# Optimization experiments

Measured on AMD Instinct MI355X. Metric: run time of the kernel, lower is better.

## Reference

```python
import jax, jax.numpy as jnp
import numpy as np

EPS = 1e-6
GROUPS = 32
SCALE = 1.0 / np.float32(512.0) ** 0.5


def setup_inputs() -> dict:
    key = jax.random.key(0)
    ks = jax.random.split(key, 8)
    b, c, h, w = 4, 512, 64, 64
    std = 0.02
    return {
        "x": jax.random.normal(ks[0], (b, c, h, w), dtype=jnp.float32),
        "gamma": jnp.ones((c,), jnp.float32),
        "beta": jnp.zeros((c,), jnp.float32),
        "wq_w": jax.random.normal(ks[1], (c, c), jnp.float32) * std,
        "wq_b": jax.random.normal(ks[2], (c,), jnp.float32) * std,
        "wk_w": jax.random.normal(ks[3], (c, c), jnp.float32) * std,
        "wk_b": jax.random.normal(ks[4], (c,), jnp.float32) * std,
        "wv_w": jax.random.normal(ks[5], (c, c), jnp.float32) * std,
        "wv_b": jax.random.normal(ks[6], (c,), jnp.float32) * std,
        "out_w": jax.random.normal(ks[7], (c, c), jnp.float32) * std,
        "out_b": jnp.zeros((c,), jnp.float32),
    }


def reference(x, gamma, beta, wq_w, wq_b, wk_w, wk_b, wv_w, wv_b, out_w, out_b):
    b, c, h, w = x.shape
    # GroupNorm(32 groups, eps=1e-6, affine)
    xg = x.reshape(b, GROUPS, c // GROUPS, h, w)
    mean = xg.mean(axis=(2, 3, 4), keepdims=True)
    var = ((xg - mean) ** 2).mean(axis=(2, 3, 4), keepdims=True)
    xn = ((xg - mean) * jax.lax.rsqrt(var + EPS)).reshape(b, c, h, w)
    xn = xn * gamma[None, :, None, None] + beta[None, :, None, None]
    # flatten spatial -> tokens: [b, N, c]
    t = xn.reshape(b, c, h * w).transpose(0, 2, 1)
    q = t @ wq_w.T + wq_b
    k = t @ wk_w.T + wk_b
    v = t @ wv_w.T + wv_b
    scores = jnp.einsum('bnc,bmc->bnm', q, k) * SCALE  # [b, N, N]
    attn = jax.nn.softmax(scores, axis=2)
    o = jnp.einsum('bnm,bmc->bnc', attn, v)
    o = o @ out_w.T + out_b
    return o.transpose(0, 2, 1).reshape(b, c, h, w) + x
```

## Files before the change

kernel.cpp:

```cpp
#include <hip/hip_runtime.h>
#include <hip/hip_fp8.h>

typedef unsigned short u16;
typedef unsigned char u8;
typedef unsigned int u32;
typedef short bf16x8 __attribute__((ext_vector_type(8)));
typedef float f32x4 __attribute__((ext_vector_type(4)));
typedef u16 u16x4 __attribute__((ext_vector_type(4)));

#define SCALE_Q 0.044194173824159216f

#define BAR() asm volatile("s_waitcnt lgkmcnt(0)\n\ts_barrier" ::: "memory")

__device__ __forceinline__ u16 f2b(float f){
  unsigned u = __float_as_uint(f);
  u += 0x7fffu + ((u >> 16) & 1u);
  return (u16)(u >> 16);
}

__device__ __forceinline__ u8 f2e4(float f){
  return __hip_fp8_e4m3(f).__x;
}

__device__ __forceinline__ void gload16(const void* g, void* l){
  __builtin_amdgcn_global_load_lds(
      (const __attribute__((address_space(1))) void*)g,
      (__attribute__((address_space(3))) void*)l, 16, 0, 0);
}

__device__ __forceinline__ float qsum16(float v){
  v += __shfl_xor(v, 1); v += __shfl_xor(v, 2);
  v += __shfl_xor(v, 4); v += __shfl_xor(v, 8);
  return v;
}

__global__ __launch_bounds__(256) void gn_stats(const float* __restrict__ x,
                                                float* __restrict__ stats){
  int bg = blockIdx.x;
  const float4* p4 = (const float4*)(x + (size_t)bg * 65536);
  float s = 0.f, ss = 0.f;
  for (int i = threadIdx.x; i < 16384; i += 256){
    float4 v = p4[i];
    s  += v.x + v.y + v.z + v.w;
    ss += v.x*v.x + v.y*v.y + v.z*v.z + v.w*v.w;
  }
  for (int off = 32; off; off >>= 1){
    s  += __shfl_down(s, off);
    ss += __shfl_down(ss, off);
  }
  __shared__ float as_[4], bs_[4];
  int wid = threadIdx.x >> 6, lid = threadIdx.x & 63;
  if (lid == 0){ as_[wid] = s; bs_[wid] = ss; }
  __syncthreads();
  if (threadIdx.x == 0){
    float S = as_[0]+as_[1]+as_[2]+as_[3], SS = bs_[0]+bs_[1]+bs_[2]+bs_[3];
    float mean = S * (1.f/65536.f);
    float var  = SS * (1.f/65536.f) - mean*mean;
    stats[2*bg]   = mean;
    stats[2*bg+1] = rsqrtf(var + 1e-6f);
  }
}

__global__ __launch_bounds__(256) void gn_apply_T(const float* __restrict__ x,
                                                  const float* __restrict__ stats,
                                                  const float* __restrict__ gamma,
                                                  const float* __restrict__ beta,
                                                  u16* __restrict__ t){
  __shared__ float tile[32][33];
  int nb = blockIdx.x, cb = blockIdx.y, b = blockIdx.z;
  int tx = threadIdx.x & 31, ty = threadIdx.x >> 5;
  int n0 = nb * 32, c0 = cb * 32;
  #pragma unroll
  for (int i = 0; i < 4; i++){
    int ch = c0 + ty + i*8;
    float mean = stats[2*((b<<5) + (ch>>4))];
    float rstd = stats[2*((b<<5) + (ch>>4)) + 1];
    float v = x[(((size_t)b*512 + ch) << 12) + n0 + tx];
    tile[ty + i*8][tx] = (v - mean) * rstd * gamma[ch] + beta[ch];
  }
  __syncthreads();
  #pragma unroll
  for (int i = 0; i < 4; i++){
    int n = n0 + ty + i*8;
    int ch = c0 + tx;
    t[((size_t)((b<<12) + n))*512 + ch] = f2b(tile[tx][ty + i*8]);
  }
}

__global__ __launch_bounds__(256) void w2bf(const float* __restrict__ a,
                                            const float* __restrict__ b,
                                            const float* __restrict__ c,
                                            const float* __restrict__ d,
                                            u16* __restrict__ o){
  int idx = blockIdx.x * 256 + threadIdx.x;
  int which = idx >> 16;
  const float4* src = (const float4*)(which == 0 ? a : which == 1 ? b : which == 2 ? c : d);
  float4 v = src[idx & 65535];
  u16x4 pk;
  pk.x = f2b(v.x); pk.y = f2b(v.y); pk.z = f2b(v.z); pk.w = f2b(v.w);
  *(u16x4*)(o + (size_t)idx*4) = pk;
}

__global__ __launch_bounds__(256, 2) void qkv_gemm(const u16* __restrict__ A,
                                                   const u16* __restrict__ Wcat,
                                                   const float* __restrict__ qbias,
                                                   const float* __restrict__ kbias,
                                                   const float* __restrict__ vbias,
                                                   u8* __restrict__ qo,
                                                   u8* __restrict__ ko,
                                                   u8* __restrict__ vo){
  __shared__ __align__(16) u16 SMEM[8192];
  u16* As = SMEM;
  u16* Bs = SMEM + 4096;
  const int t = threadIdx.x;
  const int w = t >> 6, ln = t & 63;
  const int wr = w >> 1, wc = w & 1;
  const int q4 = ln >> 4, l15 = ln & 15;
  const int y = blockIdx.y;
  const int mat = y >> 2, yb = y & 3;
  const int row0 = blockIdx.x * 128;
  const u16* Ab = A    + (size_t)row0 * 512;
  const u16* Bb = Wcat + (size_t)y * 128 * 512;
  f32x4 acc[4][4];
  #pragma unroll
  for (int i = 0; i < 4; i++)
    #pragma unroll
    for (int j = 0; j < 4; j++){
      acc[i][j][0]=0.f; acc[i][j][1]=0.f; acc[i][j][2]=0.f; acc[i][j][3]=0.f;
    }
  for (int kt = 0; kt < 16; ++kt){
    #pragma unroll
    for (int i = 0; i < 2; i++){
      int idx = i*256 + t;
      gload16(Ab + (size_t)(idx>>2)*512 + kt*32 + (idx&3)*8, As + (size_t)idx*8);
      gload16(Bb + (size_t)(idx>>2)*512 + kt*32 + (idx&3)*8, Bs + (size_t)idx*8);
    }
    __syncthreads();
    bf16x8 af[4], bf[4];
    #pragma unroll
    for (int mt = 0; mt < 4; mt++)
      af[mt] = *(const bf16x8*)(As + (wr*64 + mt*16 + l15)*32 + q4*8);
    #pragma unroll
    for (int nt = 0; nt < 4; nt++)
      bf[nt] = *(const bf16x8*)(Bs + (wc*64 + nt*16 + l15)*32 + q4*8);
    #pragma unroll
    for (int mt = 0; mt < 4; mt++)
      #pragma unroll
      for (int nt = 0; nt < 4; nt++)
        acc[mt][nt] = __builtin_amdgcn_mfma_f32_16x16x32_bf16(af[mt], bf[nt], acc[mt][nt], 0, 0, 0);
    __syncthreads();
  }
  const int bb = row0 >> 12;
  const int tile0 = (row0 >> 6) & 63;
  const int col0 = yb*128 + wc*64;
  u8* Ls = (u8*)SMEM;

  if (mat == 0){
    #pragma unroll
    for (int nt = 0; nt < 4; nt++){
      int n = col0 + nt*16 + l15;
      float bv = qbias[n];
      #pragma unroll
      for (int mt = 0; mt < 4; mt++){
        int m0 = row0 + wr*64 + mt*16 + q4*4;
        #pragma unroll
        for (int r = 0; r < 4; r++)
          qo[(size_t)(m0 + r)*512 + n] = f2e4(acc[mt][nt][r] + bv);
      }
    }
  } else if (mat == 1){
    #pragma unroll
    for (int nt = 0; nt < 4; nt++){
      int n = col0 + nt*16 + l15;
      float bv = kbias[n];
      int ksl = wc*2 + (nt >> 1);
      int c3  = ((nt & 1)*2 + (l15 >> 3));
      #pragma unroll
      for (int mt = 0; mt < 4; mt++){
        #pragma unroll
        for (int r = 0; r < 4; r++){
          int kr = mt*16 + q4*4 + r;
          int chunk = c3 ^ ((kr >> 2) & 3);
          Ls[(wr*4 + ksl)*2048 + kr*32 + chunk*8 + (l15 & 7)] = f2e4(acc[mt][nt][r] + bv);
        }
      }
    }
    __syncthreads();
    #pragma unroll
    for (int i = 0; i < 4; i++){
      int ci = i*256 + t;
      int ri = ci >> 7, t2 = ri >> 2, ksl2 = ri & 3;
      u8* dst = ko + ((size_t)(bb*64 + tile0 + t2))*32768
                   + (size_t)(yb*4 + ksl2)*2048 + (size_t)(ci & 127)*16;
      *(float4*)dst = *(const float4*)(Ls + (size_t)ci*16);
    }
  } else {
    #pragma unroll
    for (int nt = 0; nt < 4; nt++){
      int n = col0 + nt*16 + l15;
      float bv = vbias[n];
      int nl = n & 127;
      #pragma unroll
      for (int mt = 0; mt < 4; mt++){
        int kv = mt*16 + q4*4;
        u32 pk = (u32)f2e4(acc[mt][nt][0] + bv)
               | ((u32)f2e4(acc[mt][nt][1] + bv) << 8)
               | ((u32)f2e4(acc[mt][nt][2] + bv) << 16)
               | ((u32)f2e4(acc[mt][nt][3] + bv) << 24);
        int phys = (kv >> 3) ^ (n & 7);
        *(u32*)(Ls + wr*8192 + nl*64 + phys*8 + (kv & 4)) = pk;
      }
    }
    __syncthreads();
    #pragma unroll
    for (int i = 0; i < 4; i++){
      int ci = i*256 + t;
      int t2 = ci >> 9;
      u8* dst = vo + ((size_t)(bb*64 + tile0 + t2))*32768
                   + (size_t)yb*8192 + (size_t)(ci & 511)*16;
      *(float4*)dst = *(const float4*)(Ls + (size_t)ci*16);
    }
  }
}

__global__ __launch_bounds__(256, 2) void out_gemm(const u16* __restrict__ A,
                                                   const u16* __restrict__ Bw,
                                                   const float* __restrict__ bias,
                                                   float* __restrict__ out,
                                                   const float* __restrict__ resid){
  __shared__ __align__(16) u16 As[128*32];
  __shared__ __align__(16) u16 Bs[128*32];
  const int t = threadIdx.x;
  const int w = t >> 6, ln = t & 63;
  const int wr = w >> 1, wc = w & 1;
  const int q4 = ln >> 4, l15 = ln & 15;
  const u16* Ab = A  + (size_t)blockIdx.x * 128 * 512;
  const u16* Bb = Bw + (size_t)blockIdx.y * 128 * 512;
  f32x4 acc[4][4];
  #pragma unroll
  for (int i = 0; i < 4; i++)
    #pragma unroll
    for (int j = 0; j < 4; j++){
      acc[i][j][0]=0.f; acc[i][j][1]=0.f; acc[i][j][2]=0.f; acc[i][j][3]=0.f;
    }
  for (int kt = 0; kt < 16; ++kt){
    #pragma unroll
    for (int i = 0; i < 2; i++){
      int idx = i*256 + t;
      gload16(Ab + (size_t)(idx>>2)*512 + kt*32 + (idx&3)*8, As + (size_t)idx*8);
      gload16(Bb + (size_t)(idx>>2)*512 + kt*32 + (idx&3)*8, Bs + (size_t)idx*8);
    }
    __syncthreads();
    bf16x8 af[4], bf[4];
    #pragma unroll
    for (int mt = 0; mt < 4; mt++)
      af[mt] = *(const bf16x8*)(As + (wr*64 + mt*16 + l15)*32 + q4*8);
    #pragma unroll
    for (int nt = 0; nt < 4; nt++)
      bf[nt] = *(const bf16x8*)(Bs + (wc*64 + nt*16 + l15)*32 + q4*8);
    #pragma unroll
    for (int mt = 0; mt < 4; mt++)
      #pragma unroll
      for (int nt = 0; nt < 4; nt++)
        acc[mt][nt] = __builtin_amdgcn_mfma_f32_16x16x32_bf16(af[mt], bf[nt], acc[mt][nt], 0, 0, 0);
    __syncthreads();
  }
  const int row0 = blockIdx.x*128 + wr*64;
  const int col0 = blockIdx.y*128 + wc*64;
  #pragma unroll
  for (int nt = 0; nt < 4; nt++){
    int n = col0 + nt*16 + l15;
    float bv = bias[n];
    #pragma unroll
    for (int mt = 0; mt < 4; mt++){
      int m0 = row0 + mt*16 + q4*4;
      int bb = m0 >> 12, tok = m0 & 4095;
      size_t base = (((size_t)(bb*512 + n)) << 12) + tok;
      float4 xr = *(const float4*)(resid + base);
      float4 ov;
      ov.x = acc[mt][nt][0] + bv + xr.x;
      ov.y = acc[mt][nt][1] + bv + xr.y;
      ov.z = acc[mt][nt][2] + bv + xr.z;
      ov.w = acc[mt][nt][3] + bv + xr.w;
      *(float4*)(out + base) = ov;
    }
  }
}

__global__ __launch_bounds__(256, 2) void attn_fwd(const u8* __restrict__ q,
                                                   const u8* __restrict__ kt,
                                                   const u8* __restrict__ vt,
                                                   u16* __restrict__ outO){
  __shared__ __align__(16) u8 Kb[2][32768];
  __shared__ __align__(16) u8 Pb[32*72];
  __shared__ __align__(16) float lL[64];

  const int t = threadIdx.x, w = t >> 6, ln = t & 63;
  const int q4 = ln >> 4, l15 = ln & 15;
  const int rt = w >> 1, chh = w & 1;
  const int b = blockIdx.y, q0 = blockIdx.x * 32;
  const u8* kbase = kt + ((size_t)b << 21);
  const u8* vbase = vt + ((size_t)b << 21);

  long qf[16];
  {
    const u8* qr = q + (size_t)((b<<12) + q0 + rt*16 + l15) * 512;
    #pragma unroll
    for (int ks = 0; ks < 16; ks++) qf[ks] = *(const long*)(qr + ks*32 + q4*8);
  }
  f32x4 oacc[2][8];
  #pragma unroll
  for (int i = 0; i < 2; i++)
    #pragma unroll
    for (int j = 0; j < 8; j++){
      oacc[i][j][0]=0.f; oacc[i][j][1]=0.f; oacc[i][j][2]=0.f; oacc[i][j][3]=0.f;
    }
  f32x4 lrow; lrow[0]=0.f; lrow[1]=0.f; lrow[2]=0.f; lrow[3]=0.f;

  const int kr0 = chh*32 + l15,  kr1 = chh*32 + 16 + l15;
  const int ko0 = kr0*32 + ((q4 ^ ((kr0 >> 2) & 3)) << 3);
  const int ko1 = kr1*32 + ((q4 ^ ((kr1 >> 2) & 3)) << 3);

  #pragma unroll
  for (int i = 0; i < 8; i++){
    int ci = i*256 + t;
    gload16(kbase + (size_t)ci*16, &Kb[0][ci*16]);
  }
  __syncthreads();

  #pragma unroll 1
  for (int j = 0; j < 64; ++j){
    {
      const u8* kn = kbase + ((size_t)((j + 1) & 63) << 15);
      u8* kd = Kb[(j + 1) & 1];
      #pragma unroll
      for (int i = 0; i < 8; i++){
        int ci = i*256 + t;
        gload16(kn + (size_t)ci*16, kd + ci*16);
      }
    }
    long vf0[8], vf1[8];
    {
      const u8* vtile = vbase + ((size_t)j << 15);
      #pragma unroll
      for (int ct = 0; ct < 8; ct++){
        int ch = 128*w + ct*16 + l15;
        int swz = ch & 7;
        const u8* vr = vtile + (size_t)ch*64;
        vf0[ct] = *(const long*)(vr + ((q4 ^ swz) << 3));
        vf1[ct] = *(const long*)(vr + (((4 + q4) ^ swz) << 3));
      }
    }
    const u8* Kp = Kb[j & 1];
    f32x4 sA0, sA1, sB0, sB1;
    sA0[0]=0.f;sA0[1]=0.f;sA0[2]=0.f;sA0[3]=0.f;
    sA1[0]=0.f;sA1[1]=0.f;sA1[2]=0.f;sA1[3]=0.f;
    sB0[0]=0.f;sB0[1]=0.f;sB0[2]=0.f;sB0[3]=0.f;
    sB1[0]=0.f;sB1[1]=0.f;sB1[2]=0.f;sB1[3]=0.f;
    #pragma unroll
    for (int k2 = 0; k2 < 8; k2++){
      const u8* e0 = Kp + (2*k2)*2048;
      const u8* e1 = Kp + (2*k2 + 1)*2048;
      long ka0 = *(const long*)(e0 + ko0);
      long kb0 = *(const long*)(e0 + ko1);
      long ka1 = *(const long*)(e1 + ko0);
      long kb1 = *(const long*)(e1 + ko1);
      sA0 = __builtin_amdgcn_mfma_f32_16x16x32_fp8_fp8(qf[2*k2],   ka0, sA0, 0, 0, 0);
      sB0 = __builtin_amdgcn_mfma_f32_16x16x32_fp8_fp8(qf[2*k2],   kb0, sB0, 0, 0, 0);
      sA1 = __builtin_amdgcn_mfma_f32_16x16x32_fp8_fp8(qf[2*k2+1], ka1, sA1, 0, 0, 0);
      sB1 = __builtin_amdgcn_mfma_f32_16x16x32_fp8_fp8(qf[2*k2+1], kb1, sB1, 0, 0, 0);
    }
    #pragma unroll
    for (int r = 0; r < 4; r++){
      float e0 = __expf((sA0[r] + sA1[r]) * SCALE_Q);
      float e1 = __expf((sB0[r] + sB1[r]) * SCALE_Q);
      lrow[r] += e0 + e1;
      int row = rt*16 + q4*4 + r;
      Pb[row*72 + chh*32 + l15]      = f2e4(e0);
      Pb[row*72 + chh*32 + 16 + l15] = f2e4(e1);
    }
    BAR();
    {
      long pf00 = *(const long*)(Pb + l15*72 + q4*8);
      long pf01 = *(const long*)(Pb + l15*72 + 32 + q4*8);
      long pf10 = *(const long*)(Pb + (16 + l15)*72 + q4*8);
      long pf11 = *(const long*)(Pb + (16 + l15)*72 + 32 + q4*8);
      #pragma unroll
      for (int ct = 0; ct < 8; ct++){
        f32x4 a0 = oacc[0][ct], a1 = oacc[1][ct];
        a0 = __builtin_amdgcn_mfma_f32_16x16x32_fp8_fp8(pf00, vf0[ct], a0, 0, 0, 0);
        a1 = __builtin_amdgcn_mfma_f32_16x16x32_fp8_fp8(pf10, vf0[ct], a1, 0, 0, 0);
        a0 = __builtin_amdgcn_mfma_f32_16x16x32_fp8_fp8(pf01, vf1[ct], a0, 0, 0, 0);
        a1 = __builtin_amdgcn_mfma_f32_16x16x32_fp8_fp8(pf11, vf1[ct], a1, 0, 0, 0);
        oacc[0][ct] = a0; oacc[1][ct] = a1;
      }
    }
    __syncthreads();
  }

  {
    f32x4 ls;
    #pragma unroll
    for (int r = 0; r < 4; r++) ls[r] = qsum16(lrow[r]);
    if (l15 == 0) *(f32x4*)&lL[chh*32 + rt*16 + q4*4] = ls;
  }
  __syncthreads();
  #pragma unroll
  for (int rr = 0; rr < 2; rr++){
    #pragma unroll
    for (int r = 0; r < 4; r++){
      int row = rr*16 + q4*4 + r;
      float inv = 1.f / (lL[row] + lL[32 + row]);
      u16* op = outO + ((size_t)b << 21) + (size_t)(q0 + row)*512 + 128*w + l15;
      #pragma unroll
      for (int ct = 0; ct < 8; ct++)
        op[ct*16] = f2b(oacc[rr][ct][r] * inv);
    }
  }
}

extern "C" void kernel_launch(void* const* d_in, const int* in_sizes, int n_in,
                              void* d_out, int out_size, void* d_ws, size_t ws_size,
                              hipStream_t stream){
  const float* x     = (const float*)d_in[0];
  const float* gamma = (const float*)d_in[1];
  const float* beta  = (const float*)d_in[2];
  const float* wq_w  = (const float*)d_in[3];
  const float* wq_b  = (const float*)d_in[4];
  const float* wk_w  = (const float*)d_in[5];
  const float* wk_b  = (const float*)d_in[6];
  const float* wv_w  = (const float*)d_in[7];
  const float* wv_b  = (const float*)d_in[8];
  const float* out_w = (const float*)d_in[9];
  const float* out_b = (const float*)d_in[10];

  char* ws = (char*)d_ws;
  float* stats = (float*)ws;
  u16* tbuf = (u16*)(ws + 4096);
  size_t off = 4096 + (size_t)16*1024*1024;
  u16* Wcat = (u16*)(ws + off); off += (size_t)4*512*512*2;
  u8*  qb   = (u8*)(ws + off);  off += (size_t)16*1024*1024;
  u8*  ktb  = (u8*)(ws + off);  off += (size_t)16*1024*1024;
  u8*  vtb  = (u8*)(ws + off);  off += (size_t)16*1024*1024;

  gn_stats<<<128, 256, 0, stream>>>(x, stats);
  gn_apply_T<<<dim3(128, 16, 4), 256, 0, stream>>>(x, stats, gamma, beta, tbuf);
  w2bf<<<1024, 256, 0, stream>>>(wq_w, wk_w, wv_w, out_w, Wcat);
  u16* Wo = Wcat + 3*512*512;
  qkv_gemm<<<dim3(128, 12), 256, 0, stream>>>(tbuf, Wcat, wq_b, wk_b, wv_b,
                                              qb, ktb, vtb);
  attn_fwd<<<dim3(128, 4), 256, 0, stream>>>(qb, ktb, vtb, tbuf);
  out_gemm<<<dim3(128, 4), 256, 0, stream>>>(tbuf, Wo, out_b, (float*)d_out, x);
}
```

Measured before the change: 323.9 us.

## Software-pipeline attention loop: overlap PV of previous tile with QK of current

Restructures the attention inner loop into a two-stage software pipeline. The P@V product for tile j-1 runs right after the QK MFMAs for tile j, and P and V fragments are double-buffered so only one barrier per iteration remains. The loop is unrolled by two through a macro, and MFMA sections are wrapped in s_setprio raises. This aims to remove the mid-iteration barrier stall and hide exp/softmax latency behind matrix work. The cost is higher register pressure from the extra V fragment buffers, which could spill at the two-blocks-per-SM launch bound.

```diff
diff --git a/kernel.cpp b/kernel.cpp
--- a/kernel.cpp
+++ b/kernel.cpp
@@ -9,8 +9,6 @@
 typedef u16 u16x4 __attribute__((ext_vector_type(4)));
 
 #define SCALE_Q 0.044194173824159216f
-
-#define BAR() asm volatile("s_waitcnt lgkmcnt(0)\n\ts_barrier" ::: "memory")
 
 __device__ __forceinline__ u16 f2b(float f){
   unsigned u = __float_as_uint(f);
@@ -287,12 +285,84 @@
   }
 }
 
+#define AITER(J, PCUR, PPRV, VN0, VN1, VP0, VP1, KCUR, KNXT)                  \
+  {                                                                           \
+                 \
+    if ((J) < 63){                                                            \
+      const u8* kn = kbase + ((size_t)((J) + 1) << 15);                       \
+      _Pragma("unroll")                                                       \
+      for (int i = 0; i < 8; i++){                                            \
+        int ci = i*256 + t;                                                   \
+        gload16(kn + (size_t)ci*16, &Kb[KNXT][ci*16]);                        \
+      }                                                                       \
+    }                                                                         \
+        \
+    {                                                                         \
+      const u8* vtile = vbase + ((size_t)(J) << 15);                          \
+      _Pragma("unroll")                                                       \
+      for (int ct = 0; ct < 8; ct++){                                         \
+        int ch = 128*w + ct*16 + l15;                                         \
+        int swz = ch & 7;                                                     \
+        const u8* vr = vtile + (size_t)ch*64;                                 \
+        VN0[ct] = *(const long*)(vr + ((q4 ^ swz) << 3));                     \
+        VN1[ct] = *(const long*)(vr + (((4 + q4) ^ swz) << 3));               \
+      }                                                                       \
+    }                                                                         \
+                             \
+    const u8* Kp = Kb[KCUR];                                                  \
+    f32x4 sA0 = {0.f,0.f,0.f,0.f}, sA1 = {0.f,0.f,0.f,0.f};                   \
+    f32x4 sB0 = {0.f,0.f,0.f,0.f}, sB1 = {0.f,0.f,0.f,0.f};                   \
+    __builtin_amdgcn_s_setprio(1);                                            \
+    _Pragma("unroll")                                                         \
+    for (int k2 = 0; k2 < 8; k2++){                                           \
+      const u8* e0 = Kp + (2*k2)*2048;                                        \
+      const u8* e1 = Kp + (2*k2 + 1)*2048;                                    \
+      long ka0 = *(const long*)(e0 + ko0);                                    \
+      long kb0 = *(const long*)(e0 + ko1);                                    \
+      long ka1 = *(const long*)(e1 + ko0);                                    \
+      long kb1 = *(const long*)(e1 + ko1);                                    \
+      sA0 = __builtin_amdgcn_mfma_f32_16x16x32_fp8_fp8(qf[2*k2],   ka0, sA0, 0, 0, 0); \
+      sB0 = __builtin_amdgcn_mfma_f32_16x16x32_fp8_fp8(qf[2*k2],   kb0, sB0, 0, 0, 0); \
+      sA1 = __builtin_amdgcn_mfma_f32_16x16x32_fp8_fp8(qf[2*k2+1], ka1, sA1, 0, 0, 0); \
+      sB1 = __builtin_amdgcn_mfma_f32_16x16x32_fp8_fp8(qf[2*k2+1], kb1, sB1, 0, 0, 0); \
+    }                                                                         \
+      \
+    if ((J) > 0){                                                             \
+      long pf00 = *(const long*)((PPRV) + l15*72 + q4*8);                     \
+      long pf01 = *(const long*)((PPRV) + l15*72 + 32 + q4*8);                \
+      long pf10 = *(const long*)((PPRV) + (16 + l15)*72 + q4*8);              \
+      long pf11 = *(const long*)((PPRV) + (16 + l15)*72 + 32 + q4*8);         \
+      _Pragma("unroll")                                                       \
+      for (int ct = 0; ct < 8; ct++){                                         \
+        f32x4 a0 = oacc[0][ct], a1 = oacc[1][ct];                             \
+        a0 = __builtin_amdgcn_mfma_f32_16x16x32_fp8_fp8(pf00, VP0[ct], a0, 0, 0, 0); \
+        a1 = __builtin_amdgcn_mfma_f32_16x16x32_fp8_fp8(pf10, VP0[ct], a1, 0, 0, 0); \
+        a0 = __builtin_amdgcn_mfma_f32_16x16x32_fp8_fp8(pf01, VP1[ct], a0, 0, 0, 0); \
+        a1 = __builtin_amdgcn_mfma_f32_16x16x32_fp8_fp8(pf11, VP1[ct], a1, 0, 0, 0); \
+        oacc[0][ct] = a0; oacc[1][ct] = a1;                                   \
+      }                                                                       \
+    }                                                                         \
+    __builtin_amdgcn_s_setprio(0);                                            \
+              \
+    _Pragma("unroll")                                                         \
+    for (int r = 0; r < 4; r++){                                              \
+      float e0 = __expf((sA0[r] + sA1[r]) * SCALE_Q);                         \
+      float e1 = __expf((sB0[r] + sB1[r]) * SCALE_Q);                         \
+      lrow[r] += e0 + e1;                                                     \
+      int row = rt*16 + q4*4 + r;                                             \
+      (PCUR)[row*72 + chh*32 + l15]      = f2e4(e0);                          \
+      (PCUR)[row*72 + chh*32 + 16 + l15] = f2e4(e1);                          \
+    }                                                                         \
+           \
+    __syncthreads();                                                          \
+  }
+
 __global__ __launch_bounds__(256, 2) void attn_fwd(const u8* __restrict__ q,
                                                    const u8* __restrict__ kt,
                                                    const u8* __restrict__ vt,
                                                    u16* __restrict__ outO){
   __shared__ __align__(16) u8 Kb[2][32768];
-  __shared__ __align__(16) u8 Pb[32*72];
+  __shared__ __align__(16) u8 Pb[2][32*72];
   __shared__ __align__(16) float lL[64];
 
   const int t = threadIdx.x, w = t >> 6, ln = t & 63;
@@ -328,74 +398,29 @@
   }
   __syncthreads();
 
+  long vA0[8], vA1[8], vB0[8], vB1[8];
+
   #pragma unroll 1
-  for (int j = 0; j < 64; ++j){
-    {
-      const u8* kn = kbase + ((size_t)((j + 1) & 63) << 15);
-      u8* kd = Kb[(j + 1) & 1];
-      #pragma unroll
-      for (int i = 0; i < 8; i++){
-        int ci = i*256 + t;
-        gload16(kn + (size_t)ci*16, kd + ci*16);
-      }
-    }
-    long vf0[8], vf1[8];
-    {
-      const u8* vtile = vbase + ((size_t)j << 15);
-      #pragma unroll
-      for (int ct = 0; ct < 8; ct++){
-        int ch = 128*w + ct*16 + l15;
-        int swz = ch & 7;
-        const u8* vr = vtile + (size_t)ch*64;
-        vf0[ct] = *(const long*)(vr + ((q4 ^ swz) << 3));
-        vf1[ct] = *(const long*)(vr + (((4 + q4) ^ swz) << 3));
-      }
-    }
-    const u8* Kp = Kb[j & 1];
-    f32x4 sA0, sA1, sB0, sB1;
-    sA0[0]=0.f;sA0[1]=0.f;sA0[2]=0.f;sA0[3]=0.f;
-    sA1[0]=0.f;sA1[1]=0.f;sA1[2]=0.f;sA1[3]=0.f;
-    sB0[0]=0.f;sB0[1]=0.f;sB0[2]=0.f;sB0[3]=0.f;
-    sB1[0]=0.f;sB1[1]=0.f;sB1[2]=0.f;sB1[3]=0.f;
-    #pragma unroll
-    for (int k2 = 0; k2 < 8; k2++){
-      const u8* e0 = Kp + (2*k2)*2048;
-      const u8* e1 = Kp + (2*k2 + 1)*2048;
-      long ka0 = *(const long*)(e0 + ko0);
-      long kb0 = *(const long*)(e0 + ko1);
-      long ka1 = *(const long*)(e1 + ko0);
-      long kb1 = *(const long*)(e1 + ko1);
-      sA0 = __builtin_amdgcn_mfma_f32_16x16x32_fp8_fp8(qf[2*k2],   ka0, sA0, 0, 0, 0);
-      sB0 = __builtin_amdgcn_mfma_f32_16x16x32_fp8_fp8(qf[2*k2],   kb0, sB0, 0, 0, 0);
-      sA1 = __builtin_amdgcn_mfma_f32_16x16x32_fp8_fp8(qf[2*k2+1], ka1, sA1, 0, 0, 0);
-      sB1 = __builtin_amdgcn_mfma_f32_16x16x32_fp8_fp8(qf[2*k2+1], kb1, sB1, 0, 0, 0);
-    }
-    #pragma unroll
-    for (int r = 0; r < 4; r++){
-      float e0 = __expf((sA0[r] + sA1[r]) * SCALE_Q);
-      float e1 = __expf((sB0[r] + sB1[r]) * SCALE_Q);
-      lrow[r] += e0 + e1;
-      int row = rt*16 + q4*4 + r;
-      Pb[row*72 + chh*32 + l15]      = f2e4(e0);
-      Pb[row*72 + chh*32 + 16 + l15] = f2e4(e1);
-    }
-    BAR();
-    {
-      long pf00 = *(const long*)(Pb + l15*72 + q4*8);
-      long pf01 = *(const long*)(Pb + l15*72 + 32 + q4*8);
-      long pf10 = *(const long*)(Pb + (16 + l15)*72 + q4*8);
-      long pf11 = *(const long*)(Pb + (16 + l15)*72 + 32 + q4*8);
-      #pragma unroll
-      for (int ct = 0; ct < 8; ct++){
-        f32x4 a0 = oacc[0][ct], a1 = oacc[1][ct];
-        a0 = __builtin_amdgcn_mfma_f32_16x16x32_fp8_fp8(pf00, vf0[ct], a0, 0, 0, 0);
-        a1 = __builtin_amdgcn_mfma_f32_16x16x32_fp8_fp8(pf10, vf0[ct], a1, 0, 0, 0);
-        a0 = __builtin_amdgcn_mfma_f32_16x16x32_fp8_fp8(pf01, vf1[ct], a0, 0, 0, 0);
-        a1 = __builtin_amdgcn_mfma_f32_16x16x32_fp8_fp8(pf11, vf1[ct], a1, 0, 0, 0);
-        oacc[0][ct] = a0; oacc[1][ct] = a1;
-      }
-    }
-    __syncthreads();
+  for (int j = 0; j < 64; j += 2){
+    AITER(j,     Pb[0], Pb[1], vA0, vA1, vB0, vB1, 0, 1);
+    AITER(j + 1, Pb[1], Pb[0], vB0, vB1, vA0, vA1, 1, 0);
+  }
+
+  {
+    const u8* PP = Pb[1];
+    long pf00 = *(const long*)(PP + l15*72 + q4*8);
+    long pf01 = *(const long*)(PP + l15*72 + 32 + q4*8);
+    long pf10 = *(const long*)(PP + (16 + l15)*72 + q4*8);
+    long pf11 = *(const long*)(PP + (16 + l15)*72 + 32 + q4*8);
+    #pragma unroll
+    for (int ct = 0; ct < 8; ct++){
+      f32x4 a0 = oacc[0][ct], a1 = oacc[1][ct];
+      a0 = __builtin_amdgcn_mfma_f32_16x16x32_fp8_fp8(pf00, vB0[ct], a0, 0, 0, 0);
+      a1 = __builtin_amdgcn_mfma_f32_16x16x32_fp8_fp8(pf10, vB0[ct], a1, 0, 0, 0);
+      a0 = __builtin_amdgcn_mfma_f32_16x16x32_fp8_fp8(pf01, vB1[ct], a0, 0, 0, 0);
+      a1 = __builtin_amdgcn_mfma_f32_16x16x32_fp8_fp8(pf11, vB1[ct], a1, 0, 0, 0);
+      oacc[0][ct] = a0; oacc[1][ct] = a1;
+    }
   }
 
   {
```

Measured after the change: 384.4 us. 1.19x slower.

## Software-pipeline attention loop: overlap QK of tile j with PV of tile j-1

Applied to the files above, without the earlier changes.

Restructures the attention main loop so each iteration computes QK scores for the current key tile while running the PV MFMAs on the probabilities from the previous tile, using a double-buffered P array in LDS. This removes one of the two barriers per iteration and lets exp/softmax work overlap MFMA work from another stage. A tail block handles the last PV tile, and s_setprio raises wave priority around the MFMA section. The trade-off is higher register pressure from holding V fragments and score accumulators together, plus a slightly larger LDS footprint.

```diff
diff --git a/kernel.cpp b/kernel.cpp
--- a/kernel.cpp
+++ b/kernel.cpp
@@ -9,8 +9,6 @@
 typedef u16 u16x4 __attribute__((ext_vector_type(4)));
 
 #define SCALE_Q 0.044194173824159216f
-
-#define BAR() asm volatile("s_waitcnt lgkmcnt(0)\n\ts_barrier" ::: "memory")
 
 __device__ __forceinline__ u16 f2b(float f){
   unsigned u = __float_as_uint(f);
@@ -292,7 +290,7 @@
                                                    const u8* __restrict__ vt,
                                                    u16* __restrict__ outO){
   __shared__ __align__(16) u8 Kb[2][32768];
-  __shared__ __align__(16) u8 Pb[32*72];
+  __shared__ __align__(16) u8 Pb[2][32*72];
   __shared__ __align__(16) float lL[64];
 
   const int t = threadIdx.x, w = t >> 6, ln = t & 63;
@@ -330,8 +328,8 @@
 
   #pragma unroll 1
   for (int j = 0; j < 64; ++j){
-    {
-      const u8* kn = kbase + ((size_t)((j + 1) & 63) << 15);
+    if (j < 63){
+      const u8* kn = kbase + ((size_t)(j + 1) << 15);
       u8* kd = Kb[(j + 1) & 1];
       #pragma unroll
       for (int i = 0; i < 8; i++){
@@ -340,8 +338,8 @@
       }
     }
     long vf0[8], vf1[8];
-    {
-      const u8* vtile = vbase + ((size_t)j << 15);
+    if (j > 0){
+      const u8* vtile = vbase + ((size_t)(j - 1) << 15);
       #pragma unroll
       for (int ct = 0; ct < 8; ct++){
         int ch = 128*w + ct*16 + l15;
@@ -357,6 +355,7 @@
     sA1[0]=0.f;sA1[1]=0.f;sA1[2]=0.f;sA1[3]=0.f;
     sB0[0]=0.f;sB0[1]=0.f;sB0[2]=0.f;sB0[3]=0.f;
     sB1[0]=0.f;sB1[1]=0.f;sB1[2]=0.f;sB1[3]=0.f;
+    __builtin_amdgcn_s_setprio(1);
     #pragma unroll
     for (int k2 = 0; k2 < 8; k2++){
       const u8* e0 = Kp + (2*k2)*2048;
@@ -370,21 +369,12 @@
       sA1 = __builtin_amdgcn_mfma_f32_16x16x32_fp8_fp8(qf[2*k2+1], ka1, sA1, 0, 0, 0);
       sB1 = __builtin_amdgcn_mfma_f32_16x16x32_fp8_fp8(qf[2*k2+1], kb1, sB1, 0, 0, 0);
     }
-    #pragma unroll
-    for (int r = 0; r < 4; r++){
-      float e0 = __expf((sA0[r] + sA1[r]) * SCALE_Q);
-      float e1 = __expf((sB0[r] + sB1[r]) * SCALE_Q);
-      lrow[r] += e0 + e1;
-      int row = rt*16 + q4*4 + r;
-      Pb[row*72 + chh*32 + l15]      = f2e4(e0);
-      Pb[row*72 + chh*32 + 16 + l15] = f2e4(e1);
-    }
-    BAR();
-    {
-      long pf00 = *(const long*)(Pb + l15*72 + q4*8);
-      long pf01 = *(const long*)(Pb + l15*72 + 32 + q4*8);
-      long pf10 = *(const long*)(Pb + (16 + l15)*72 + q4*8);
-      long pf11 = *(const long*)(Pb + (16 + l15)*72 + 32 + q4*8);
+    if (j > 0){
+      const u8* Pp = Pb[(j - 1) & 1];
+      long pf00 = *(const long*)(Pp + l15*72 + q4*8);
+      long pf01 = *(const long*)(Pp + l15*72 + 32 + q4*8);
+      long pf10 = *(const long*)(Pp + (16 + l15)*72 + q4*8);
+      long pf11 = *(const long*)(Pp + (16 + l15)*72 + 32 + q4*8);
       #pragma unroll
       for (int ct = 0; ct < 8; ct++){
         f32x4 a0 = oacc[0][ct], a1 = oacc[1][ct];
@@ -395,7 +385,44 @@
         oacc[0][ct] = a0; oacc[1][ct] = a1;
       }
     }
-    __syncthreads();
+    __builtin_amdgcn_s_setprio(0);
+    #pragma unroll
+    for (int r = 0; r < 4; r++){
+      float e0 = __expf((sA0[r] + sA1[r]) * SCALE_Q);
+      float e1 = __expf((sB0[r] + sB1[r]) * SCALE_Q);
+      lrow[r] += e0 + e1;
+      int row = rt*16 + q4*4 + r;
+      Pb[j & 1][row*72 + chh*32 + l15]      = f2e4(e0);
+      Pb[j & 1][row*72 + chh*32 + 16 + l15] = f2e4(e1);
+    }
+    __syncthreads();
+  }
+
+  {
+    const u8* vtile = vbase + ((size_t)63 << 15);
+    long vf0[8], vf1[8];
+    #pragma unroll
+    for (int ct = 0; ct < 8; ct++){
+      int ch = 128*w + ct*16 + l15;
+      int swz = ch & 7;
+      const u8* vr = vtile + (size_t)ch*64;
+      vf0[ct] = *(const long*)(vr + ((q4 ^ swz) << 3));
+      vf1[ct] = *(const long*)(vr + (((4 + q4) ^ swz) << 3));
+    }
+    const u8* Pp = Pb[1];
+    long pf00 = *(const long*)(Pp + l15*72 + q4*8);
+    long pf01 = *(const long*)(Pp + l15*72 + 32 + q4*8);
+    long pf10 = *(const long*)(Pp + (16 + l15)*72 + q4*8);
+    long pf11 = *(const long*)(Pp + (16 + l15)*72 + 32 + q4*8);
+    #pragma unroll
+    for (int ct = 0; ct < 8; ct++){
+      f32x4 a0 = oacc[0][ct], a1 = oacc[1][ct];
+      a0 = __builtin_amdgcn_mfma_f32_16x16x32_fp8_fp8(pf00, vf0[ct], a0, 0, 0, 0);
+      a1 = __builtin_amdgcn_mfma_f32_16x16x32_fp8_fp8(pf10, vf0[ct], a1, 0, 0, 0);
+      a0 = __builtin_amdgcn_mfma_f32_16x16x32_fp8_fp8(pf01, vf1[ct], a0, 0, 0, 0);
+      a1 = __builtin_amdgcn_mfma_f32_16x16x32_fp8_fp8(pf11, vf1[ct], a1, 0, 0, 0);
+      oacc[0][ct] = a0; oacc[1][ct] = a1;
+    }
   }
 
   {
```

Measured after the change: 338.0 us. 4.4% more time.

## Warp-specialize attention into score and PV wave groups with software pipelining

Applied to the files above, without the earlier changes.

The attention kernel moves to 512 threads and splits them into two roles. Four waves compute QK^T scores and exp for the current 128-key tile, and four waves run the PV MFMAs for the previous tile from a double-buffered P tile, so softmax and the two matmuls overlap across tiles. K tiles double in size to 64 KB per buffer, which halves the loop trip count. P is packed to fp8 four values at a time with cvt_pk, and s_setprio is raised around MFMA bursts. In exchange the kernel uses much more LDS (about 137 KB), which may limit occupancy to one block per CU despite the launch bound of two, and the two roles can become imbalanced.

```diff
diff --git a/kernel.cpp b/kernel.cpp
--- a/kernel.cpp
+++ b/kernel.cpp
@@ -10,8 +10,6 @@
 
 #define SCALE_Q 0.044194173824159216f
 
-#define BAR() asm volatile("s_waitcnt lgkmcnt(0)\n\ts_barrier" ::: "memory")
-
 __device__ __forceinline__ u16 f2b(float f){
   unsigned u = __float_as_uint(f);
   u += 0x7fffu + ((u >> 16) & 1u);
@@ -22,16 +20,21 @@
   return __hip_fp8_e4m3(f).__x;
 }
 
+__device__ __forceinline__ u32 pk4e4(float e0, float e1, float e2, float e3){
+#if defined(__has_builtin) && __has_builtin(__builtin_amdgcn_cvt_pk_fp8_f32)
+  int pk = __builtin_amdgcn_cvt_pk_fp8_f32(e0, e1, 0, false);
+  pk = __builtin_amdgcn_cvt_pk_fp8_f32(e2, e3, pk, true);
+  return (u32)pk;
+#else
+  return (u32)f2e4(e0) | ((u32)f2e4(e1) << 8)
+       | ((u32)f2e4(e2) << 16) | ((u32)f2e4(e3) << 24);
+#endif
+}
+
 __device__ __forceinline__ void gload16(const void* g, void* l){
   __builtin_amdgcn_global_load_lds(
       (const __attribute__((address_space(1))) void*)g,
       (__attribute__((address_space(3))) void*)l, 16, 0, 0);
-}
-
-__device__ __forceinline__ float qsum16(float v){
-  v += __shfl_xor(v, 1); v += __shfl_xor(v, 2);
-  v += __shfl_xor(v, 4); v += __shfl_xor(v, 8);
-  return v;
 }
 
 __global__ __launch_bounds__(256) void gn_stats(const float* __restrict__ x,
@@ -287,134 +290,210 @@
   }
 }
 
-__global__ __launch_bounds__(256, 2) void attn_fwd(const u8* __restrict__ q,
+#define PSTR 140
+__global__ __launch_bounds__(512, 2) void attn_fwd(const u8* __restrict__ q,
                                                    const u8* __restrict__ kt,
                                                    const u8* __restrict__ vt,
                                                    u16* __restrict__ outO){
-  __shared__ __align__(16) u8 Kb[2][32768];
-  __shared__ __align__(16) u8 Pb[32*72];
+  __shared__ __align__(16) u8 Kb[2][65536];
+  __shared__ __align__(16) u8 Pb[2][32*PSTR];
   __shared__ __align__(16) float lL[64];
 
   const int t = threadIdx.x, w = t >> 6, ln = t & 63;
   const int q4 = ln >> 4, l15 = ln & 15;
-  const int rt = w >> 1, chh = w & 1;
   const int b = blockIdx.y, q0 = blockIdx.x * 32;
   const u8* kbase = kt + ((size_t)b << 21);
   const u8* vbase = vt + ((size_t)b << 21);
+  const bool isS = (w < 4);
+  const int rt = w & 1, kvH = w >> 1;
+  const int wp = w & 3, ch0 = wp * 128;
 
   long qf[16];
-  {
+  int ko0, ko1, ko2, ko3;
+  float lrow = 0.f;
+  if (isS){
     const u8* qr = q + (size_t)((b<<12) + q0 + rt*16 + l15) * 512;
     #pragma unroll
     for (int ks = 0; ks < 16; ks++) qf[ks] = *(const long*)(qr + ks*32 + q4*8);
-  }
+    int kr0 = 0*16 + l15, kr1 = 1*16 + l15, kr2 = 2*16 + l15, kr3 = 3*16 + l15;
+    ko0 = kr0*32 + ((q4 ^ ((kr0 >> 2) & 3)) << 3);
+    ko1 = kr1*32 + ((q4 ^ ((kr1 >> 2) & 3)) << 3);
+    ko2 = kr2*32 + ((q4 ^ ((kr2 >> 2) & 3)) << 3);
+    ko3 = kr3*32 + ((q4 ^ ((kr3 >> 2) & 3)) << 3);
+  }
+
   f32x4 oacc[2][8];
-  #pragma unroll
-  for (int i = 0; i < 2; i++)
-    #pragma unroll
-    for (int j = 0; j < 8; j++){
-      oacc[i][j][0]=0.f; oacc[i][j][1]=0.f; oacc[i][j][2]=0.f; oacc[i][j][3]=0.f;
-    }
-  f32x4 lrow; lrow[0]=0.f; lrow[1]=0.f; lrow[2]=0.f; lrow[3]=0.f;
-
-  const int kr0 = chh*32 + l15,  kr1 = chh*32 + 16 + l15;
-  const int ko0 = kr0*32 + ((q4 ^ ((kr0 >> 2) & 3)) << 3);
-  const int ko1 = kr1*32 + ((q4 ^ ((kr1 >> 2) & 3)) << 3);
+  int vo0[8], vo1[8];
+  if (!isS){
+    #pragma unroll
+    for (int i = 0; i < 2; i++)
+      #pragma unroll
+      for (int j = 0; j < 8; j++){
+        oacc[i][j][0]=0.f; oacc[i][j][1]=0.f; oacc[i][j][2]=0.f; oacc[i][j][3]=0.f;
+      }
+    #pragma unroll
+    for (int ct = 0; ct < 8; ct++){
+      int ch = ch0 + ct*16 + l15;
+      int swz = ch & 7;
+      vo0[ct] = ch*64 + ((q4 ^ swz) << 3);
+      vo1[ct] = ch*64 + (((4 + q4) ^ swz) << 3);
+    }
+  }
 
   #pragma unroll
   for (int i = 0; i < 8; i++){
-    int ci = i*256 + t;
+    int ci = i*512 + t;
     gload16(kbase + (size_t)ci*16, &Kb[0][ci*16]);
   }
   __syncthreads();
 
   #pragma unroll 1
-  for (int j = 0; j < 64; ++j){
-    {
-      const u8* kn = kbase + ((size_t)((j + 1) & 63) << 15);
+  for (int j = 0; j < 32; ++j){
+    if (j < 31){
+      const u8* kn = kbase + ((size_t)(j + 1) << 16);
       u8* kd = Kb[(j + 1) & 1];
       #pragma unroll
       for (int i = 0; i < 8; i++){
-        int ci = i*256 + t;
+        int ci = i*512 + t;
         gload16(kn + (size_t)ci*16, kd + ci*16);
       }
     }
-    long vf0[8], vf1[8];
-    {
-      const u8* vtile = vbase + ((size_t)j << 15);
+    if (isS){
+      const u8* Kp = &Kb[j & 1][kvH * 32768];
+      f32x4 s0, s1, s2, s3;
+      s0[0]=0.f;s0[1]=0.f;s0[2]=0.f;s0[3]=0.f;
+      s1[0]=0.f;s1[1]=0.f;s1[2]=0.f;s1[3]=0.f;
+      s2[0]=0.f;s2[1]=0.f;s2[2]=0.f;s2[3]=0.f;
+      s3[0]=0.f;s3[1]=0.f;s3[2]=0.f;s3[3]=0.f;
+      __builtin_amdgcn_s_setprio(1);
+      #pragma unroll
+      for (int ks = 0; ks < 16; ks++){
+        const u8* e = Kp + ks*2048;
+        long k0 = *(const long*)(e + ko0);
+        long k1 = *(const long*)(e + ko1);
+        long k2 = *(const long*)(e + ko2);
+        long k3 = *(const long*)(e + ko3);
+        long qv = qf[ks];
+        s0 = __builtin_amdgcn_mfma_f32_16x16x32_fp8_fp8(k0, qv, s0, 0, 0, 0);
+        s1 = __builtin_amdgcn_mfma_f32_16x16x32_fp8_fp8(k1, qv, s1, 0, 0, 0);
+        s2 = __builtin_amdgcn_mfma_f32_16x16x32_fp8_fp8(k2, qv, s2, 0, 0, 0);
+        s3 = __builtin_amdgcn_mfma_f32_16x16x32_fp8_fp8(k3, qv, s3, 0, 0, 0);
+      }
+      __builtin_amdgcn_s_setprio(0);
+      u8* Pw = Pb[j & 1] + (rt*16 + l15)*PSTR + kvH*64 + q4*4;
+      {
+        float e0 = __expf(s0[0]*SCALE_Q), e1 = __expf(s0[1]*SCALE_Q);
+        float e2 = __expf(s0[2]*SCALE_Q), e3 = __expf(s0[3]*SCALE_Q);
+        lrow += (e0+e1)+(e2+e3);
+        *(u32*)(Pw) = pk4e4(e0, e1, e2, e3);
+        e0 = __expf(s1[0]*SCALE_Q); e1 = __expf(s1[1]*SCALE_Q);
+        e2 = __expf(s1[2]*SCALE_Q); e3 = __expf(s1[3]*SCALE_Q);
+        lrow += (e0+e1)+(e2+e3);
+        *(u32*)(Pw + 16) = pk4e4(e0, e1, e2, e3);
+        e0 = __expf(s2[0]*SCALE_Q); e1 = __expf(s2[1]*SCALE_Q);
+        e2 = __expf(s2[2]*SCALE_Q); e3 = __expf(s2[3]*SCALE_Q);
+        lrow += (e0+e1)+(e2+e3);
+        *(u32*)(Pw + 32) = pk4e4(e0, e1, e2, e3);
+        e0 = __expf(s3[0]*SCALE_Q); e1 = __expf(s3[1]*SCALE_Q);
+        e2 = __expf(s3[2]*SCALE_Q); e3 = __expf(s3[3]*SCALE_Q);
+        lrow += (e0+e1)+(e2+e3);
+        *(u32*)(Pw + 48) = pk4e4(e0, e1, e2, e3);
+      }
+    } else if (j > 0){
+      const u8* vtA = vbase + ((size_t)(j - 1) << 16);
+      const u8* vtB = vtA + 32768;
+      long vA0[8], vA1[8], vB0[8], vB1[8];
       #pragma unroll
       for (int ct = 0; ct < 8; ct++){
-        int ch = 128*w + ct*16 + l15;
-        int swz = ch & 7;
-        const u8* vr = vtile + (size_t)ch*64;
-        vf0[ct] = *(const long*)(vr + ((q4 ^ swz) << 3));
-        vf1[ct] = *(const long*)(vr + (((4 + q4) ^ swz) << 3));
-      }
-    }
-    const u8* Kp = Kb[j & 1];
-    f32x4 sA0, sA1, sB0, sB1;
-    sA0[0]=0.f;sA0[1]=0.f;sA0[2]=0.f;sA0[3]=0.f;
-    sA1[0]=0.f;sA1[1]=0.f;sA1[2]=0.f;sA1[3]=0.f;
-    sB0[0]=0.f;sB0[1]=0.f;sB0[2]=0.f;sB0[3]=0.f;
-    sB1[0]=0.f;sB1[1]=0.f;sB1[2]=0.f;sB1[3]=0.f;
-    #pragma unroll
-    for (int k2 = 0; k2 < 8; k2++){
-      const u8* e0 = Kp + (2*k2)*2048;
-      const u8* e1 = Kp + (2*k2 + 1)*2048;
-      long ka0 = *(const long*)(e0 + ko0);
-      long kb0 = *(const long*)(e0 + ko1);
-      long ka1 = *(const long*)(e1 + ko0);
-      long kb1 = *(const long*)(e1 + ko1);
-      sA0 = __builtin_amdgcn_mfma_f32_16x16x32_fp8_fp8(qf[2*k2],   ka0, sA0, 0, 0, 0);
-      sB0 = __builtin_amdgcn_mfma_f32_16x16x32_fp8_fp8(qf[2*k2],   kb0, sB0, 0, 0, 0);
-      sA1 = __builtin_amdgcn_mfma_f32_16x16x32_fp8_fp8(qf[2*k2+1], ka1, sA1, 0, 0, 0);
-      sB1 = __builtin_amdgcn_mfma_f32_16x16x32_fp8_fp8(qf[2*k2+1], kb1, sB1, 0, 0, 0);
-    }
-    #pragma unroll
-    for (int r = 0; r < 4; r++){
-      float e0 = __expf((sA0[r] + sA1[r]) * SCALE_Q);
-      float e1 = __expf((sB0[r] + sB1[r]) * SCALE_Q);
-      lrow[r] += e0 + e1;
-      int row = rt*16 + q4*4 + r;
-      Pb[row*72 + chh*32 + l15]      = f2e4(e0);
-      Pb[row*72 + chh*32 + 16 + l15] = f2e4(e1);
-    }
-    BAR();
-    {
-      long pf00 = *(const long*)(Pb + l15*72 + q4*8);
-      long pf01 = *(const long*)(Pb + l15*72 + 32 + q4*8);
-      long pf10 = *(const long*)(Pb + (16 + l15)*72 + q4*8);
-      long pf11 = *(const long*)(Pb + (16 + l15)*72 + 32 + q4*8);
+        vA0[ct] = *(const long*)(vtA + vo0[ct]);
+        vA1[ct] = *(const long*)(vtA + vo1[ct]);
+        vB0[ct] = *(const long*)(vtB + vo0[ct]);
+        vB1[ct] = *(const long*)(vtB + vo1[ct]);
+      }
+      const u8* Pp = Pb[(j - 1) & 1];
+      const u8* p0 = Pp + l15*PSTR;
+      const u8* p1 = Pp + (16 + l15)*PSTR;
+      long pA0a = *(const long*)(p0 + q4*8);
+      long pA1a = *(const long*)(p0 + 32 + q4*8);
+      long pB0a = *(const long*)(p0 + 64 + q4*8);
+      long pB1a = *(const long*)(p0 + 96 + q4*8);
+      long pA0b = *(const long*)(p1 + q4*8);
+      long pA1b = *(const long*)(p1 + 32 + q4*8);
+      long pB0b = *(const long*)(p1 + 64 + q4*8);
+      long pB1b = *(const long*)(p1 + 96 + q4*8);
+      __builtin_amdgcn_s_setprio(1);
       #pragma unroll
       for (int ct = 0; ct < 8; ct++){
         f32x4 a0 = oacc[0][ct], a1 = oacc[1][ct];
-        a0 = __builtin_amdgcn_mfma_f32_16x16x32_fp8_fp8(pf00, vf0[ct], a0, 0, 0, 0);
-        a1 = __builtin_amdgcn_mfma_f32_16x16x32_fp8_fp8(pf10, vf0[ct], a1, 0, 0, 0);
-        a0 = __builtin_amdgcn_mfma_f32_16x16x32_fp8_fp8(pf01, vf1[ct], a0, 0, 0, 0);
-        a1 = __builtin_amdgcn_mfma_f32_16x16x32_fp8_fp8(pf11, vf1[ct], a1, 0, 0, 0);
+        a0 = __builtin_amdgcn_mfma_f32_16x16x32_fp8_fp8(pA0a, vA0[ct], a0, 0, 0, 0);
+        a1 = __builtin_amdgcn_mfma_f32_16x16x32_fp8_fp8(pA0b, vA0[ct], a1, 0, 0, 0);
+        a0 = __builtin_amdgcn_mfma_f32_16x16x32_fp8_fp8(pA1a, vA1[ct], a0, 0, 0, 0);
+        a1 = __builtin_amdgcn_mfma_f32_16x16x32_fp8_fp8(pA1b, vA1[ct], a1, 0, 0, 0);
+        a0 = __builtin_amdgcn_mfma_f32_16x16x32_fp8_fp8(pB0a, vB0[ct], a0, 0, 0, 0);
+        a1 = __builtin_amdgcn_mfma_f32_16x16x32_fp8_fp8(pB0b, vB0[ct], a1, 0, 0, 0);
+        a0 = __builtin_amdgcn_mfma_f32_16x16x32_fp8_fp8(pB1a, vB1[ct], a0, 0, 0, 0);
+        a1 = __builtin_amdgcn_mfma_f32_16x16x32_fp8_fp8(pB1b, vB1[ct], a1, 0, 0, 0);
         oacc[0][ct] = a0; oacc[1][ct] = a1;
       }
-    }
-    __syncthreads();
-  }
-
-  {
-    f32x4 ls;
-    #pragma unroll
-    for (int r = 0; r < 4; r++) ls[r] = qsum16(lrow[r]);
-    if (l15 == 0) *(f32x4*)&lL[chh*32 + rt*16 + q4*4] = ls;
+      __builtin_amdgcn_s_setprio(0);
+    }
+    __syncthreads();
+  }
+
+  if (isS){
+    float v = lrow;
+    v += __shfl_xor(v, 16);
+    v += __shfl_xor(v, 32);
+    if (ln < 16) lL[kvH*32 + rt*16 + ln] = v;
+  } else {
+    const u8* vtA = vbase + ((size_t)31 << 16);
+    const u8* vtB = vtA + 32768;
+    long vA0[8], vA1[8], vB0[8], vB1[8];
+    #pragma unroll
+    for (int ct = 0; ct < 8; ct++){
+      vA0[ct] = *(const long*)(vtA + vo0[ct]);
+      vA1[ct] = *(const long*)(vtA + vo1[ct]);
+      vB0[ct] = *(const long*)(vtB + vo0[ct]);
+      vB1[ct] = *(const long*)(vtB + vo1[ct]);
+    }
+    const u8* Pp = Pb[1];
+    const u8* p0 = Pp + l15*PSTR;
+    const u8* p1 = Pp + (16 + l15)*PSTR;
+    long pA0a = *(const long*)(p0 + q4*8);
+    long pA1a = *(const long*)(p0 + 32 + q4*8);
+    long pB0a = *(const long*)(p0 + 64 + q4*8);
+    long pB1a = *(const long*)(p0 + 96 + q4*8);
+    long pA0b = *(const long*)(p1 + q4*8);
+    long pA1b = *(const long*)(p1 + 32 + q4*8);
+    long pB0b = *(const long*)(p1 + 64 + q4*8);
+    long pB1b = *(const long*)(p1 + 96 + q4*8);
+    #pragma unroll
+    for (int ct = 0; ct < 8; ct++){
+      f32x4 a0 = oacc[0][ct], a1 = oacc[1][ct];
+      a0 = __builtin_amdgcn_mfma_f32_16x16x32_fp8_fp8(pA0a, vA0[ct], a0, 0, 0, 0);
+      a1 = __builtin_amdgcn_mfma_f32_16x16x32_fp8_fp8(pA0b, vA0[ct], a1, 0, 0, 0);
+      a0 = __builtin_amdgcn_mfma_f32_16x16x32_fp8_fp8(pA1a, vA1[ct], a0, 0, 0, 0);
+      a1 = __builtin_amdgcn_mfma_f32_16x16x32_fp8_fp8(pA1b, vA1[ct], a1, 0, 0, 0);
+      a0 = __builtin_amdgcn_mfma_f32_16x16x32_fp8_fp8(pB0a, vB0[ct], a0, 0, 0, 0);
+      a1 = __builtin_amdgcn_mfma_f32_16x16x32_fp8_fp8(pB0b, vB0[ct], a1, 0, 0, 0);
+      a0 = __builtin_amdgcn_mfma_f32_16x16x32_fp8_fp8(pB1a, vB1[ct], a0, 0, 0, 0);
+      a1 = __builtin_amdgcn_mfma_f32_16x16x32_fp8_fp8(pB1b, vB1[ct], a1, 0, 0, 0);
+      oacc[0][ct] = a0; oacc[1][ct] = a1;
+    }
   }
   __syncthreads();
-  #pragma unroll
-  for (int rr = 0; rr < 2; rr++){
-    #pragma unroll
-    for (int r = 0; r < 4; r++){
-      int row = rr*16 + q4*4 + r;
-      float inv = 1.f / (lL[row] + lL[32 + row]);
-      u16* op = outO + ((size_t)b << 21) + (size_t)(q0 + row)*512 + 128*w + l15;
-      #pragma unroll
-      for (int ct = 0; ct < 8; ct++)
-        op[ct*16] = f2b(oacc[rr][ct][r] * inv);
+  if (!isS){
+    #pragma unroll
+    for (int rr = 0; rr < 2; rr++){
+      #pragma unroll
+      for (int r = 0; r < 4; r++){
+        int row = rr*16 + q4*4 + r;
+        float inv = 1.f / (lL[row] + lL[32 + row]);
+        u16* op = outO + ((size_t)b << 21) + (size_t)(q0 + row)*512 + ch0 + l15;
+        #pragma unroll
+        for (int ct = 0; ct < 8; ct++)
+          op[ct*16] = f2b(oacc[rr][ct][r] * inv);
+      }
     }
   }
 }
@@ -449,6 +528,6 @@
   u16* Wo = Wcat + 3*512*512;
   qkv_gemm<<<dim3(128, 12), 256, 0, stream>>>(tbuf, Wcat, wq_b, wk_b, wv_b,
                                               qb, ktb, vtb);
-  attn_fwd<<<dim3(128, 4), 256, 0, stream>>>(qb, ktb, vtb, tbuf);
+  attn_fwd<<<dim3(128, 4), 512, 0, stream>>>(qb, ktb, vtb, tbuf);
   out_gemm<<<dim3(128, 4), 256, 0, stream>>>(tbuf, Wo, out_b, (float*)d_out, x);
 }
```

Result: slower. 379.0 us (+17.0%).
